# Kernel optimization log

Measured on AMD Instinct MI355X. Metric: run time of the kernel, lower is better.

Reference implementation:

```python
import jax, jax.numpy as jnp
import numpy as np

NUM_HEADS = 8


def setup_inputs() -> dict:
    key = jax.random.key(0)
    ks = jax.random.split(key, 7)
    B, D, N = 16, 512, 2048
    sc = 1.0 / np.sqrt(D)
    return {
        "X_Query": jax.random.normal(ks[0], (B, D, N), jnp.float32),
        "X_Key": jax.random.normal(ks[1], (B, D, N), jnp.float32),
        "X_Value": jax.random.normal(ks[2], (B, D, N), jnp.float32),
        "W_q": jax.random.normal(ks[3], (D, D), jnp.float32) * sc,
        "W_k": jax.random.normal(ks[4], (D, D), jnp.float32) * sc,
        "W_v": jax.random.normal(ks[5], (D, D), jnp.float32) * sc,
        "W_o": jax.random.normal(ks[6], (D, D), jnp.float32) * sc,
    }


def _proj(W, x):
    # Conv1d(D, D, kernel_size=1, bias=False) == channel matmul
    return jnp.einsum('oi,bin->bon', W, x)


def _split_heads(x, h):
    # torch: cat(x.chunk(h, dim=-1), dim=0) -> (h, B, D, N/h) stacked layout
    B, D, N = x.shape
    return x.reshape(B, D, h, N // h).transpose(2, 0, 1, 3)


def _mha(XQ, XK, XV, Wq, Wk, Wv, Wo):
    B, D, N = XQ.shape
    h = NUM_HEADS
    Nh = N // h
    q = _split_heads(_proj(Wq, XQ), h)  # (h, B, D, Nh)
    k = _split_heads(_proj(Wk, XK), h)
    v = _split_heads(_proj(Wv, XV), h)
    # scores over the CHANNEL axis: (h, B, D, D), scaled by sqrt(d_k)=sqrt(Nh)
    scores = jnp.einsum('hbdn,hben->hbde', q, k) / jnp.sqrt(jnp.asarray(Nh, q.dtype))
    p = jax.nn.softmax(scores, axis=-1)
    out = jnp.einsum('hbde,hben->hbdn', p, v)  # (h, B, D, Nh)
    # torch: cat(chunks, dim=0) inverse -> cat along dim=-1
    attn_heads = out.transpose(1, 2, 0, 3).reshape(B, D, N)
    return _proj(Wo, XQ - attn_heads)


def reference(X_Query, X_Key, X_Value, W_q, W_k, W_v, W_o):
    return _mha(X_Query, X_Key, X_Value, W_q, W_k, W_v, W_o)
```

## Files before the change

### kernel.cpp

```cpp
#include <hip/hip_runtime.h>
#include <hip/hip_bf16.h>

#define DD  512
#define NN  2048
#define BB  16
#define NHD 256

typedef unsigned short u16;
typedef __attribute__((ext_vector_type(4))) float f32x4;
typedef __attribute__((ext_vector_type(8))) short s16x8;
typedef __attribute__((ext_vector_type(4))) u16   u16x4;

static __device__ __forceinline__ u16 f2bf(float f) {
  __hip_bfloat16 h = __float2bfloat16(f);
  return *reinterpret_cast<u16*>(&h);
}
static __device__ __forceinline__ float bf2f(u16 u) {
  union { unsigned int i; float f; } v; v.i = ((unsigned int)u) << 16; return v.f;
}
static __device__ __forceinline__ f32x4 mfma_bf16(s16x8 a, s16x8 b, f32x4 c) {
  return __builtin_amdgcn_mfma_f32_16x16x32_bf16(a, b, c, 0, 0, 0);
}
static __device__ __forceinline__ void gload_lds16(const u16* g, u16* l) {
  __builtin_amdgcn_global_load_lds(
      (const __attribute__((address_space(1))) unsigned int*)g,
      (__attribute__((address_space(3))) unsigned int*)l, 16, 0, 0);
}

__global__ __launch_bounds__(256) void k_cvt_w(const float* __restrict__ w0,
                                               const float* __restrict__ w1,
                                               const float* __restrict__ w2,
                                               const float* __restrict__ w3,
                                               u16* __restrict__ out) {
  const float* srcs[4] = {w0, w1, w2, w3};
  const float* s = srcs[blockIdx.y];
  u16* o = out + (size_t)blockIdx.y * (DD * DD);
  int idx = blockIdx.x * 256 + threadIdx.x;
  float4 v = *(const float4*)(s + (size_t)idx * 4);
  u16x4 u = {f2bf(v.x), f2bf(v.y), f2bf(v.z), f2bf(v.w)};
  *(u16x4*)(o + (size_t)idx * 4) = u;
}

__global__ __launch_bounds__(256) void k_transpose(const float* __restrict__ X,
                                                   u16* __restrict__ XT) {
  __shared__ float t[64][68];
  const int tid = threadIdx.x;
  const int n0 = blockIdx.x * 64, d0 = blockIdx.y * 64, b = blockIdx.z;
  const float* Xb = X + ((size_t)b * DD + d0) * NN + n0;
#pragma unroll
  for (int i = 0; i < 4; ++i) {
    int r = (tid >> 4) + i * 16;
    int c = (tid & 15) * 4;
    float4 v = *(const float4*)(Xb + (size_t)r * NN + c);
    t[r][c] = v.x; t[r][c + 1] = v.y; t[r][c + 2] = v.z; t[r][c + 3] = v.w;
  }
  __syncthreads();
  u16* Ob = XT + ((size_t)b * NN + n0) * DD + d0;
#pragma unroll
  for (int i = 0; i < 4; ++i) {
    int n = (tid >> 4) + i * 16;
    int d = (tid & 15) * 4;
    u16x4 u = {f2bf(t[d][n]), f2bf(t[d + 1][n]), f2bf(t[d + 2][n]), f2bf(t[d + 3][n])};
    *(u16x4*)(Ob + (size_t)n * DD + d) = u;
  }
}

#define GEMM_STAGE(Ag, lda, Bg, ldb, buf, kt)                                   \
  {                                                                             \
    _Pragma("unroll")                                                           \
    for (int j = 0; j < 4; ++j) {                                               \
      int s = j * 256 + w * 64 + lane;                                          \
      int row = s >> 3, u = s & 7;                                              \
      int col = ((u ^ (row & 7)) * 8);                                          \
      gload_lds16(Ag + (size_t)row * lda + (kt) * 64 + col, &Ab[buf][s * 8]);   \
      gload_lds16(Bg + (size_t)row * ldb + (kt) * 64 + col, &Bb[buf][s * 8]);   \
    }                                                                           \
  }

#define GEMM_COMPUTE(buf)                                                       \
  {                                                                             \
    _Pragma("unroll")                                                           \
    for (int ks = 0; ks < 2; ++ks) {                                            \
      s16x8 av[4], bv[4];                                                       \
      _Pragma("unroll")                                                         \
      for (int m = 0; m < 4; ++m) {                                             \
        int row = wm + m * 16 + r;                                              \
        av[m] = *(const s16x8*)&Ab[buf][row * 64 + (((ks * 4 + g) ^ (row & 7)) * 8)]; \
      }                                                                         \
      _Pragma("unroll")                                                         \
      for (int nf = 0; nf < 4; ++nf) {                                          \
        int row = wn + nf * 16 + r;                                             \
        bv[nf] = *(const s16x8*)&Bb[buf][row * 64 + (((ks * 4 + g) ^ (row & 7)) * 8)]; \
      }                                                                         \
      _Pragma("unroll")                                                         \
      for (int m = 0; m < 4; ++m)                                               \
        _Pragma("unroll")                                                       \
        for (int nf = 0; nf < 4; ++nf)                                          \
          acc[m][nf] = mfma_bf16(av[m], bv[nf], acc[m][nf]);                    \
    }                                                                           \
  }

#define GEMM_PREAMBLE                                                           \
  __shared__ __align__(16) u16 Ab[2][128 * 64];                                 \
  __shared__ __align__(16) u16 Bb[2][128 * 64];                                 \
  const int tid = threadIdx.x;                                                  \
  const int lane = tid & 63, w = tid >> 6;                                      \
  const int wm = (w >> 1) * 64, wn = (w & 1) * 64;                              \
  const int r = lane & 15, g = lane >> 4;                                       \
  f32x4 acc[4][4] = {};

#define GEMM_MAINLOOP(Ag, lda, Bg, ldb, nkt)                                    \
  GEMM_STAGE(Ag, lda, Bg, ldb, 0, 0);                                           \
  __syncthreads();                                                              \
  for (int kt = 0; kt < (nkt) - 1; ++kt) {                                      \
    GEMM_STAGE(Ag, lda, Bg, ldb, (kt & 1) ^ 1, kt + 1);                         \
    GEMM_COMPUTE(kt & 1);                                                       \
    __syncthreads();                                                            \
  }                                                                             \
  GEMM_COMPUTE(((nkt) - 1) & 1);

template <typename OUT_T>
__global__ __launch_bounds__(256) void k_gemm_nt(
    const u16* __restrict__ A, long long a_bs, int lda,
    const u16* __restrict__ B, long long b_bs, int ldb,
    OUT_T* __restrict__ C, long long c_bs, int ldc, int K) {
  GEMM_PREAMBLE
  const int m0 = blockIdx.x * 128, n0 = blockIdx.y * 128;
  const u16* Ag = A + (size_t)blockIdx.z * a_bs + (size_t)m0 * lda;
  const u16* Bg = B + (size_t)blockIdx.z * b_bs + (size_t)n0 * ldb;
  const int nkt = K >> 6;
  GEMM_MAINLOOP(Ag, lda, Bg, ldb, nkt);

  OUT_T* Cg = C + (size_t)blockIdx.z * c_bs;
#pragma unroll
  for (int m = 0; m < 4; ++m)
#pragma unroll
    for (int nf = 0; nf < 4; ++nf)
#pragma unroll
      for (int j = 0; j < 4; ++j) {
        int row = m0 + wm + m * 16 + g * 4 + j;
        int col = n0 + wn + nf * 16 + r;
        float v = acc[m][nf][j];
        if constexpr (sizeof(OUT_T) == 2) Cg[(size_t)row * ldc + col] = f2bf(v);
        else                              Cg[(size_t)row * ldc + col] = v;
      }
}

__global__ __launch_bounds__(512, 2) void k_attn_fused(
    const u16* __restrict__ Qdn, const u16* __restrict__ Kdn,
    const u16* __restrict__ VT,  const u16* __restrict__ XqT,
    u16* __restrict__ And) {
  __shared__ __align__(16) u16 Ks[2][128 * 64];
  __shared__ __align__(16) u16 Vs[2][256 * 64];
  __shared__ __align__(16) u16 Ps[128 * 128];
  __shared__ float rs_lds[8][32];
  __shared__ float rs_inv[128];

  const int tid = threadIdx.x;
  const int lane = tid & 63, w = tid >> 6;
  const int r = lane & 15, g = lane >> 4;
  const int wq = w >> 1, wn1 = w & 1;
  const int bid = blockIdx.x;
  const int h = bid & 7, dt = (bid >> 3) & 3, b = bid >> 5;
  const int d0 = dt * 128, hn0 = h * NHD;

  const u16* Qg = Qdn + ((size_t)b * DD + d0) * NN + hn0;
  const u16* Kg = Kdn + ((size_t)b * DD) * NN + hn0;
  const u16* Vg = VT + ((size_t)b * NN + hn0) * DD;
  u16* Qst = (u16*)Vs;

  auto stage_k = [&](int idx) {
    const int et = idx >> 2, ks = idx & 3, buf = idx & 1;
#pragma unroll
    for (int j = 0; j < 2; ++j) {
      int s = j * 512 + tid;
      int row = s >> 3, u = s & 7;
      gload_lds16(Kg + (size_t)(et * 128 + row) * NN + ks * 64 + ((u ^ (row & 7)) * 8),
                  &Ks[buf][s * 8]);
    }
  };
  auto stage_v = [&](int et, int vs) {
#pragma unroll
    for (int j = 0; j < 4; ++j) {
      int s = j * 512 + tid;
      int row = s >> 3, u = s & 7;
      gload_lds16(Vg + (size_t)row * DD + et * 128 + vs * 64 + ((u ^ (row & 7)) * 8),
                  &Vs[vs][s * 8]);
    }
  };

  stage_k(0);
#pragma unroll
  for (int j = 0; j < 8; ++j) {
    int s = j * 512 + tid;
    int row = s >> 5, u = s & 31;
    gload_lds16(Qg + (size_t)row * NN + ((u ^ (row & 7)) * 8), &Qst[s * 8]);
  }
  __syncthreads();
  s16x8 qf[2][8];
#pragma unroll
  for (int ms = 0; ms < 2; ++ms)
#pragma unroll
    for (int k2 = 0; k2 < 8; ++k2) {
      int row = wq * 32 + ms * 16 + r;
      qf[ms][k2] = *(const s16x8*)&Qst[row * 256 + (((k2 * 4 + g) ^ (row & 7)) * 8)];
    }
  __syncthreads();

  float psum[2][4] = {};
  f32x4 acc_o[4][4] = {};

  for (int et = 0; et < 4; ++et) {
    f32x4 acc_s[2][4] = {};
#pragma unroll
    for (int ks = 0; ks < 4; ++ks) {
      const int idx = et * 4 + ks;
      if (idx + 1 < 16) stage_k(idx + 1);
      if (ks == 2) stage_v(et, 0);
      if (ks == 3) stage_v(et, 1);
      const int buf = idx & 1;
#pragma unroll
      for (int kq = 0; kq < 2; ++kq) {
        s16x8 bv[4];
#pragma unroll
        for (int nf = 0; nf < 4; ++nf) {
          int row = wn1 * 64 + nf * 16 + r;
          bv[nf] = *(const s16x8*)&Ks[buf][row * 64 + (((kq * 4 + g) ^ (row & 7)) * 8)];
        }
#pragma unroll
        for (int ms = 0; ms < 2; ++ms)
#pragma unroll
          for (int nf = 0; nf < 4; ++nf)
            acc_s[ms][nf] = mfma_bf16(qf[ms][ks * 2 + kq], bv[nf], acc_s[ms][nf]);
      }
      __syncthreads();
    }
#pragma unroll
    for (int ms = 0; ms < 2; ++ms)
#pragma unroll
      for (int nf = 0; nf < 4; ++nf)
#pragma unroll
        for (int j = 0; j < 4; ++j) {
          int rowd = wq * 32 + ms * 16 + g * 4 + j;
          int cole = wn1 * 64 + nf * 16 + r;
          float p = __expf(acc_s[ms][nf][j] * 0.0625f);
          psum[ms][j] += p;
          *(u16*)((char*)Ps + rowd * 256 + ((cole * 2) ^ ((rowd & 7) << 4))) = f2bf(p);
        }
    __syncthreads();
#pragma unroll
    for (int vs = 0; vs < 2; ++vs) {
#pragma unroll
      for (int kss = 0; kss < 2; ++kss) {
        s16x8 pb[4];
#pragma unroll
        for (int nf = 0; nf < 4; ++nf) {
          int rowd = wn1 * 64 + nf * 16 + r;
          pb[nf] = *(const s16x8*)((char*)Ps + rowd * 256 +
                                   (((vs * 64 + kss * 32 + g * 8) * 2) ^ ((rowd & 7) << 4)));
        }
#pragma unroll
        for (int ms = 0; ms < 4; ++ms) {
          int rown = wq * 64 + ms * 16 + r;
          s16x8 av = *(const s16x8*)&Vs[vs][rown * 64 + (((kss * 4 + g) ^ (rown & 7)) * 8)];
#pragma unroll
          for (int nf = 0; nf < 4; ++nf)
            acc_o[ms][nf] = mfma_bf16(av, pb[nf], acc_o[ms][nf]);
        }
      }
    }
  }

#pragma unroll
  for (int ms = 0; ms < 2; ++ms)
#pragma unroll
    for (int j = 0; j < 4; ++j) {
      float v = psum[ms][j];
      v += __shfl_xor(v, 1);
      v += __shfl_xor(v, 2);
      v += __shfl_xor(v, 4);
      v += __shfl_xor(v, 8);
      if (r == 0) rs_lds[w][ms * 16 + g * 4 + j] = v;
    }
  __syncthreads();
  if (tid < 128) {
    int q = tid >> 5, idx = tid & 31;
    rs_inv[tid] = 1.0f / (rs_lds[q * 2][idx] + rs_lds[q * 2 + 1][idx]);
  }
  __syncthreads();

  const u16* Xg = XqT + ((size_t)b * NN + hn0) * DD + d0;
  u16* Ag = And + ((size_t)b * NN + hn0) * DD + d0;
#pragma unroll
  for (int ms = 0; ms < 4; ++ms)
#pragma unroll
    for (int nf = 0; nf < 4; ++nf) {
      const int dc = wn1 * 64 + nf * 16 + r;
      const float inv = rs_inv[dc];
#pragma unroll
      for (int j = 0; j < 4; ++j) {
        const int npos = wq * 64 + ms * 16 + g * 4 + j;
        float o = acc_o[ms][nf][j] * inv;
        float xq = bf2f(Xg[(size_t)npos * DD + dc]);
        Ag[(size_t)npos * DD + dc] = f2bf(xq - o);
      }
    }
}

extern "C" void kernel_launch(void* const* d_in, const int* in_sizes, int n_in,
                              void* d_out, int out_size, void* d_ws, size_t ws_size,
                              hipStream_t stream) {
  const float* Xq = (const float*)d_in[0];
  const float* Xk = (const float*)d_in[1];
  const float* Xv = (const float*)d_in[2];
  const float* Wq = (const float*)d_in[3];
  const float* Wk = (const float*)d_in[4];
  const float* Wv = (const float*)d_in[5];
  const float* Wo = (const float*)d_in[6];
  float* out = (float*)d_out;

  char* ws = (char*)d_ws;
  const size_t MB = 1024 * 1024;
  u16* Wb  = (u16*)ws;
  u16* XqT = (u16*)(ws + 2 * MB);
  u16* Z2  = (u16*)(ws + 34 * MB);
  u16* And = Z2;
  u16* Qdn = (u16*)(ws + 66 * MB);
  u16* VTb = (u16*)d_out;
  u16* Kdn = (u16*)d_out + (size_t)BB * NN * DD;

  k_cvt_w<<<dim3(256, 4), 256, 0, stream>>>(Wq, Wk, Wv, Wo, Wb);

  k_transpose<<<dim3(NN / 64, DD / 64, BB), 256, 0, stream>>>(Xv, Z2);
  k_gemm_nt<u16><<<dim3(NN / 128, DD / 128, BB), 256, 0, stream>>>(
      Z2, (long long)NN * DD, DD,
      Wb + 2 * DD * DD, 0, DD,
      VTb, (long long)NN * DD, DD, DD);

  k_transpose<<<dim3(NN / 64, DD / 64, BB), 256, 0, stream>>>(Xq, XqT);
  k_gemm_nt<u16><<<dim3(DD / 128, NN / 128, BB), 256, 0, stream>>>(
      Wb, 0, DD,
      XqT, (long long)NN * DD, DD,
      Qdn, (long long)DD * NN, NN, DD);

  k_transpose<<<dim3(NN / 64, DD / 64, BB), 256, 0, stream>>>(Xk, Z2);
  k_gemm_nt<u16><<<dim3(DD / 128, NN / 128, BB), 256, 0, stream>>>(
      Wb + 1 * DD * DD, 0, DD,
      Z2, (long long)NN * DD, DD,
      Kdn, (long long)DD * NN, NN, DD);

  k_attn_fused<<<dim3(512), 512, 0, stream>>>(Qdn, Kdn, VTb, XqT, And);

  k_gemm_nt<float><<<dim3(DD / 128, NN / 128, BB), 256, 0, stream>>>(
      Wb + 3 * DD * DD, 0, DD,
      And, (long long)NN * DD, DD,
      out, (long long)DD * NN, NN, DD);
}
```

Baseline: 264.9 us.

## Halve attention d-tile to 64 rows, double blocks, raise occupancy

The fused channel-attention kernel now handles 64 query channels per block instead of 128. This doubles the grid to 1024 blocks, shrinks LDS to a single 72KB buffer, and raises launch bounds to 4 blocks per CU. K and V are staged in smaller double-buffered tiles with new swizzles, and per-wave accumulators shrink. The aim is more parallelism and latency hiding, at the cost of re-reading K and V twice as often and running more barriers per unit of work.

After: 255.0 us. 1.04x faster.

```diff
diff --git a/kernel.cpp b/kernel.cpp
--- a/kernel.cpp
+++ b/kernel.cpp
@@ -146,146 +146,135 @@
       }
 }
 
-__global__ __launch_bounds__(512, 2) void k_attn_fused(
+__global__ __launch_bounds__(512, 4) void k_attn_fused(
     const u16* __restrict__ Qdn, const u16* __restrict__ Kdn,
     const u16* __restrict__ VT,  const u16* __restrict__ XqT,
     u16* __restrict__ And) {
-  __shared__ __align__(16) u16 Ks[2][128 * 64];
-  __shared__ __align__(16) u16 Vs[2][256 * 64];
-  __shared__ __align__(16) u16 Ps[128 * 128];
-  __shared__ float rs_lds[8][32];
-  __shared__ float rs_inv[128];
+  __shared__ __align__(16) u16 L[36864];
+  u16* Ks = L;
+  u16* Vs = L + 16384;
+  u16* Ps = L + 32768;
 
   const int tid = threadIdx.x;
   const int lane = tid & 63, w = tid >> 6;
   const int r = lane & 15, g = lane >> 4;
-  const int wq = w >> 1, wn1 = w & 1;
+  const int dq = w >> 1, eh = w & 1;
+  const int nq = w >> 1, dh = w & 1;
   const int bid = blockIdx.x;
-  const int h = bid & 7, dt = (bid >> 3) & 3, b = bid >> 5;
-  const int d0 = dt * 128, hn0 = h * NHD;
+  const int dt = bid >> 7, hb = bid & 127;
+  const int h = hb & 7, b = hb >> 3;
+  const int d0 = dt * 64, hn0 = h * NHD;
 
   const u16* Qg = Qdn + ((size_t)b * DD + d0) * NN + hn0;
   const u16* Kg = Kdn + ((size_t)b * DD) * NN + hn0;
   const u16* Vg = VT + ((size_t)b * NN + hn0) * DD;
-  u16* Qst = (u16*)Vs;
 
   auto stage_k = [&](int idx) {
-    const int et = idx >> 2, ks = idx & 3, buf = idx & 1;
+    const int e0 = (idx >> 1) * 64, c0 = (idx & 1) * 128;
+    u16* dst = Ks + (idx & 1) * 8192;
 #pragma unroll
     for (int j = 0; j < 2; ++j) {
       int s = j * 512 + tid;
-      int row = s >> 3, u = s & 7;
-      gload_lds16(Kg + (size_t)(et * 128 + row) * NN + ks * 64 + ((u ^ (row & 7)) * 8),
-                  &Ks[buf][s * 8]);
+      int row = s >> 4, u = s & 15;
+      gload_lds16(Kg + (size_t)(e0 + row) * NN + c0 + ((u ^ (row & 7)) * 8), dst + s * 8);
     }
   };
-  auto stage_v = [&](int et, int vs) {
-#pragma unroll
-    for (int j = 0; j < 4; ++j) {
+  auto stage_v = [&](int t) {
+    u16* dst = Vs + (t & 1) * 8192;
+#pragma unroll
+    for (int j = 0; j < 2; ++j) {
       int s = j * 512 + tid;
-      int row = s >> 3, u = s & 7;
-      gload_lds16(Vg + (size_t)row * DD + et * 128 + vs * 64 + ((u ^ (row & 7)) * 8),
-                  &Vs[vs][s * 8]);
+      int row = s >> 2, u = s & 3;
+      gload_lds16(Vg + (size_t)row * DD + t * 32 + ((u ^ ((row >> 1) & 3)) * 8), dst + s * 8);
     }
   };
 
   stage_k(0);
 #pragma unroll
-  for (int j = 0; j < 8; ++j) {
+  for (int j = 0; j < 4; ++j) {
     int s = j * 512 + tid;
     int row = s >> 5, u = s & 31;
-    gload_lds16(Qg + (size_t)row * NN + ((u ^ (row & 7)) * 8), &Qst[s * 8]);
-  }
-  __syncthreads();
-  s16x8 qf[2][8];
-#pragma unroll
-  for (int ms = 0; ms < 2; ++ms)
-#pragma unroll
-    for (int k2 = 0; k2 < 8; ++k2) {
-      int row = wq * 32 + ms * 16 + r;
-      qf[ms][k2] = *(const s16x8*)&Qst[row * 256 + (((k2 * 4 + g) ^ (row & 7)) * 8)];
-    }
-  __syncthreads();
-
-  float psum[2][4] = {};
-  f32x4 acc_o[4][4] = {};
-
-  for (int et = 0; et < 4; ++et) {
-    f32x4 acc_s[2][4] = {};
-#pragma unroll
-    for (int ks = 0; ks < 4; ++ks) {
-      const int idx = et * 4 + ks;
+    gload_lds16(Qg + (size_t)row * NN + ((u ^ (row & 7)) * 8), Vs + s * 8);
+  }
+  __syncthreads();
+  s16x8 qf[8];
+#pragma unroll
+  for (int k2 = 0; k2 < 8; ++k2) {
+    int row = dq * 16 + r;
+    qf[k2] = *(const s16x8*)&Vs[row * 256 + (((k2 * 4 + g) ^ (row & 7)) * 8)];
+  }
+  __syncthreads();
+
+  float psum[4] = {};
+  f32x4 acc_o[4][2] = {};
+
+  for (int et = 0; et < 8; ++et) {
+    f32x4 acc_s[2] = {};
+#pragma unroll
+    for (int nsub = 0; nsub < 2; ++nsub) {
+      const int idx = et * 2 + nsub;
       if (idx + 1 < 16) stage_k(idx + 1);
-      if (ks == 2) stage_v(et, 0);
-      if (ks == 3) stage_v(et, 1);
-      const int buf = idx & 1;
-#pragma unroll
-      for (int kq = 0; kq < 2; ++kq) {
-        s16x8 bv[4];
-#pragma unroll
-        for (int nf = 0; nf < 4; ++nf) {
-          int row = wn1 * 64 + nf * 16 + r;
-          bv[nf] = *(const s16x8*)&Ks[buf][row * 64 + (((kq * 4 + g) ^ (row & 7)) * 8)];
+      stage_v(idx);
+      const u16* kb = Ks + (idx & 1) * 8192;
+#pragma unroll
+      for (int kq = 0; kq < 4; ++kq) {
+        s16x8 bv[2];
+#pragma unroll
+        for (int nf = 0; nf < 2; ++nf) {
+          int rowe = eh * 32 + nf * 16 + r;
+          bv[nf] = *(const s16x8*)&kb[rowe * 128 + (((kq * 4 + g) ^ (rowe & 7)) * 8)];
         }
-#pragma unroll
-        for (int ms = 0; ms < 2; ++ms)
-#pragma unroll
-          for (int nf = 0; nf < 4; ++nf)
-            acc_s[ms][nf] = mfma_bf16(qf[ms][ks * 2 + kq], bv[nf], acc_s[ms][nf]);
+        acc_s[0] = mfma_bf16(qf[nsub * 4 + kq], bv[0], acc_s[0]);
+        acc_s[1] = mfma_bf16(qf[nsub * 4 + kq], bv[1], acc_s[1]);
       }
       __syncthreads();
     }
 #pragma unroll
-    for (int ms = 0; ms < 2; ++ms)
-#pragma unroll
-      for (int nf = 0; nf < 4; ++nf)
-#pragma unroll
-        for (int j = 0; j < 4; ++j) {
-          int rowd = wq * 32 + ms * 16 + g * 4 + j;
-          int cole = wn1 * 64 + nf * 16 + r;
-          float p = __expf(acc_s[ms][nf][j] * 0.0625f);
-          psum[ms][j] += p;
-          *(u16*)((char*)Ps + rowd * 256 + ((cole * 2) ^ ((rowd & 7) << 4))) = f2bf(p);
-        }
+    for (int nf = 0; nf < 2; ++nf)
+#pragma unroll
+      for (int j = 0; j < 4; ++j) {
+        int rowd = dq * 16 + g * 4 + j;
+        int cole = eh * 32 + nf * 16 + r;
+        float p = __expf(acc_s[nf][j] * 0.0625f);
+        psum[j] += p;
+        *(u16*)((char*)Ps + rowd * 128 + (((cole >> 3) ^ (rowd & 7)) * 16) +
+                (cole & 7) * 2) = f2bf(p);
+      }
     __syncthreads();
 #pragma unroll
     for (int vs = 0; vs < 2; ++vs) {
-#pragma unroll
-      for (int kss = 0; kss < 2; ++kss) {
-        s16x8 pb[4];
-#pragma unroll
-        for (int nf = 0; nf < 4; ++nf) {
-          int rowd = wn1 * 64 + nf * 16 + r;
-          pb[nf] = *(const s16x8*)((char*)Ps + rowd * 256 +
-                                   (((vs * 64 + kss * 32 + g * 8) * 2) ^ ((rowd & 7) << 4)));
-        }
-#pragma unroll
-        for (int ms = 0; ms < 4; ++ms) {
-          int rown = wq * 64 + ms * 16 + r;
-          s16x8 av = *(const s16x8*)&Vs[vs][rown * 64 + (((kss * 4 + g) ^ (rown & 7)) * 8)];
-#pragma unroll
-          for (int nf = 0; nf < 4; ++nf)
-            acc_o[ms][nf] = mfma_bf16(av, pb[nf], acc_o[ms][nf]);
-        }
-      }
-    }
-  }
-
-#pragma unroll
-  for (int ms = 0; ms < 2; ++ms)
-#pragma unroll
-    for (int j = 0; j < 4; ++j) {
-      float v = psum[ms][j];
-      v += __shfl_xor(v, 1);
-      v += __shfl_xor(v, 2);
-      v += __shfl_xor(v, 4);
-      v += __shfl_xor(v, 8);
-      if (r == 0) rs_lds[w][ms * 16 + g * 4 + j] = v;
-    }
-  __syncthreads();
-  if (tid < 128) {
-    int q = tid >> 5, idx = tid & 31;
-    rs_inv[tid] = 1.0f / (rs_lds[q * 2][idx] + rs_lds[q * 2 + 1][idx]);
+      s16x8 pb[2];
+#pragma unroll
+      for (int nf = 0; nf < 2; ++nf) {
+        int rowd = dh * 32 + nf * 16 + r;
+        pb[nf] = *(const s16x8*)((char*)Ps + rowd * 128 + (((vs * 4 + g) ^ (rowd & 7)) * 16));
+      }
+      const u16* vb = Vs + ((et * 2 + vs) & 1) * 8192;
+#pragma unroll
+      for (int ms = 0; ms < 4; ++ms) {
+        int rown = nq * 64 + ms * 16 + r;
+        s16x8 av = *(const s16x8*)&vb[rown * 32 + ((g ^ ((rown >> 1) & 3)) * 8)];
+        acc_o[ms][0] = mfma_bf16(av, pb[0], acc_o[ms][0]);
+        acc_o[ms][1] = mfma_bf16(av, pb[1], acc_o[ms][1]);
+      }
+    }
+    __syncthreads();
+  }
+
+  float* rs = (float*)L;
+#pragma unroll
+  for (int j = 0; j < 4; ++j) {
+    float v = psum[j];
+    v += __shfl_xor(v, 1);
+    v += __shfl_xor(v, 2);
+    v += __shfl_xor(v, 4);
+    v += __shfl_xor(v, 8);
+    if (r == 0) rs[w * 16 + g * 4 + j] = v;
+  }
+  __syncthreads();
+  if (tid < 64) {
+    int dqi = tid >> 4, i = tid & 15;
+    rs[128 + tid] = 1.0f / (rs[(dqi * 2) * 16 + i] + rs[(dqi * 2 + 1) * 16 + i]);
   }
   __syncthreads();
 
@@ -294,15 +283,15 @@
 #pragma unroll
   for (int ms = 0; ms < 4; ++ms)
 #pragma unroll
-    for (int nf = 0; nf < 4; ++nf) {
-      const int dc = wn1 * 64 + nf * 16 + r;
-      const float inv = rs_inv[dc];
+    for (int nf = 0; nf < 2; ++nf) {
+      const int cold = dh * 32 + nf * 16 + r;
+      const float inv = rs[128 + cold];
 #pragma unroll
       for (int j = 0; j < 4; ++j) {
-        const int npos = wq * 64 + ms * 16 + g * 4 + j;
+        const int npos = nq * 64 + ms * 16 + g * 4 + j;
         float o = acc_o[ms][nf][j] * inv;
-        float xq = bf2f(Xg[(size_t)npos * DD + dc]);
-        Ag[(size_t)npos * DD + dc] = f2bf(xq - o);
+        float xq = bf2f(Xg[(size_t)npos * DD + cold]);
+        Ag[(size_t)npos * DD + cold] = f2bf(xq - o);
       }
     }
 }
@@ -349,7 +338,7 @@
       Z2, (long long)NN * DD, DD,
       Kdn, (long long)DD * NN, NN, DD);
 
-  k_attn_fused<<<dim3(512), 512, 0, stream>>>(Qdn, Kdn, VTb, XqT, And);
+  k_attn_fused<<<dim3(1024), 512, 0, stream>>>(Qdn, Kdn, VTb, XqT, And);
 
   k_gemm_nt<float><<<dim3(DD / 128, NN / 128, BB), 256, 0, stream>>>(
       Wb + 3 * DD * DD, 0, DD,
```
